# Optimization experiments

Hardware: AMD Instinct MI355X
Metric: run time of the kernel (lower is better)

The kernel has to match this reference:

```python
import jax, jax.numpy as jnp
import numpy as np

SIGMAS = (1.0, 10.0, 100.0, 1000.0)
EPS_RATIO = 1e-3  # lambda ridge term and ratio clip epsilon


def euclidsq(x, y):
    # squared pairwise Euclidean distances, [m, n]
    d = jnp.sum(x * x, axis=-1)[:, None] + jnp.sum(y * y, axis=-1)[None, :] - 2.0 * (x @ y.T)
    return jnp.maximum(d, 0.0)


def kmm_ratio(Kdede, Kdenu, lam):
    # original: inv(Kdede + lam*I) @ Kdenu @ ones == solve(A, Kdenu @ ones)
    n_de = Kdede.shape[0]
    A = Kdede + lam * jnp.eye(n_de, dtype=Kdede.dtype)
    B = jnp.sum(Kdenu, axis=1, keepdims=True)  # [n_de, 1]
    return jnp.linalg.solve(A, B)


def estimate_ratio(x_de, x_nu):
    # averaged KMM ratio over Gaussian kernels with fixed sigmas, then clip
    dsq_dede = euclidsq(x_de, x_de)
    dsq_denu = euclidsq(x_de, x_nu)
    ratio = 0.0
    for s in SIGMAS:
        inv2s2 = 1.0 / (2.0 * s * s)
        Kdede = jnp.exp(-dsq_dede * inv2s2)
        Kdenu = jnp.exp(-dsq_denu * inv2s2)
        ratio = ratio + kmm_ratio(Kdede, Kdenu, EPS_RATIO)
    ratio = ratio / len(SIGMAS)
    return jax.nn.relu(ratio) + EPS_RATIO  # clip_ratio=True


def reference(z1, z2, perm1, perm2):
    n, d = z1.shape
    z1s, z2s = z1[perm1], z2[perm2]
    # numerator ratio over full concatenated embeddings
    num_ratio = estimate_ratio(jnp.concatenate([z1, z2], axis=-1),
                               jnp.concatenate([z1s, z2s], axis=-1))
    num_ratio = 1.0 / num_ratio  # [n, 1]
    x_nu = jnp.concatenate([z2, z2], axis=-1)  # constant across samples

    def per_sample(z1_i):
        # x_de row j = concat(z1_i, z2_shuffled[j])
        x_de = jnp.concatenate([jnp.broadcast_to(z1_i, (n, d)), z2s], axis=-1)
        return jnp.sum(estimate_ratio(x_de, x_nu))

    denum_sums = jax.vmap(per_sample)(z1)  # [n]
    loss = jnp.sum(-jnp.log(num_ratio[:, 0] / denum_sums))
    return loss


def setup_inputs() -> dict:
    key = jax.random.key(0)
    k1, k2 = jax.random.split(key)
    n, d = 256, 128
    z1 = jax.random.normal(k1, (n, d), dtype=jnp.float32)
    z2 = jax.random.normal(k2, (n, d), dtype=jnp.float32)
    perm1 = jnp.arange(n, dtype=jnp.int32)
    perm2 = jnp.arange(n, dtype=jnp.int32)
    return {"z1": z1, "z2": z2, "perm1": perm1, "perm2": perm2}
```

## Files before the change

### kernel.cpp

```cpp
#include <hip/hip_runtime.h>
#include <math.h>

#define N 256
#define Dd 128

__device__ __forceinline__ double inv2s2_of(int s){
    return (s==0)?0.5:(s==1)?5.0e-3:(s==2)?5.0e-5:5.0e-7;
}

__device__ __forceinline__ void sweep32(double P[32][33], int tid){
    if (tid < 64){
        int r = tid & 31, cg_ = tid >> 5;
        for (int j = 0; j < 32; j++){
            double d    = P[j][j];
            double invd = 1.0 / d;
            double cr   = P[r][j];
            double s    = cr * invd;
            bool rj = (r == j);
            double nv[16];
            #pragma unroll
            for (int c = 0; c < 16; c++){
                int col = cg_*16 + c;
                double pj = P[j][col];
                double v  = P[r][col];
                nv[c] = rj ? ((col == j) ? -invd : v * invd)
                           : ((col == j) ? s : v - s*pj);
            }
            #pragma unroll
            for (int c = 0; c < 16; c++) P[r][cg_*16+c] = nv[c];
        }
        #pragma unroll
        for (int c = 0; c < 16; c++) P[r][cg_*16+c] = -P[r][cg_*16+c];
    }
}

__global__ void k_dist(const float* __restrict__ z1, const float* __restrict__ z2,
                       const int* __restrict__ p1, const int* __restrict__ p2,
                       double* __restrict__ S0, float* __restrict__ M4,
                       float* __restrict__ U4, double* __restrict__ bpart){
    __shared__ float Xs[16][17], Ys[16][17];
    int w = blockIdx.z;
    int tx = threadIdx.x, ty = threadIdx.y;
    int row = blockIdx.y*16 + ty, col = blockIdx.x*16 + tx;
    const float *Xb[2], *Yb[2]; const int *Xp[2], *Yp[2]; int npair = 1;
    Xb[1]=0; Yb[1]=0; Xp[0]=0; Yp[0]=0; Xp[1]=0; Yp[1]=0;
    switch(w){
        case 0: Xb[0]=z1; Yb[0]=z1; Xb[1]=z2; Yb[1]=z2; npair=2; break;
        case 1: Xb[0]=z1; Yb[0]=z1; Yp[0]=p1; Xb[1]=z2; Yb[1]=z2; Yp[1]=p2; npair=2; break;
        case 2: Xb[0]=z2; Yb[0]=z2; Xp[0]=p2; Yp[0]=p2; break;
        case 3: Xb[0]=z2; Yb[0]=z2; Xp[0]=p2; break;
        default:Xb[0]=z1; Yb[0]=z2; break;
    }
    double acc = 0.0;
    for (int p = 0; p < npair; p++){
        const float* X = Xb[p]; const float* Y = Yb[p];
        int xr = blockIdx.y*16 + ty; if (Xp[p]) xr = Xp[p][xr];
        int yr = blockIdx.x*16 + ty; if (Yp[p]) yr = Yp[p][yr];
        for (int c = 0; c < Dd; c += 16){
            __syncthreads();
            Xs[ty][tx] = X[xr*Dd + c + tx];
            Ys[ty][tx] = Y[yr*Dd + c + tx];
            __syncthreads();
            #pragma unroll
            for (int t = 0; t < 16; t++){
                float d = Xs[ty][t] - Ys[tx][t];
                acc += (double)d * (double)d;
            }
        }
    }
    int o = row*N + col;
    if (w == 0){
        #pragma unroll
        for (int s = 0; s < 4; s++){
            double v = exp(-inv2s2_of(s)*acc);
            if (row == col) v += 1.0e-3;
            S0[(size_t)(4+s)*N*N + o] = v;
        }
    } else if (w == 1){
        #pragma unroll
        for (int s = 0; s < 4; s++){
            double v = exp(-inv2s2_of(s)*acc);
            v += __shfl_down(v, 8, 16);
            v += __shfl_down(v, 4, 16);
            v += __shfl_down(v, 2, 16);
            v += __shfl_down(v, 1, 16);
            if (tx == 0) bpart[((size_t)s*N + row)*16 + blockIdx.x] = v;
        }
    } else if (w == 2){
        #pragma unroll
        for (int s = 0; s < 4; s++){
            double v = exp(-inv2s2_of(s)*acc);
            if (row == col) v += 1.0e-3;
            S0[(size_t)s*N*N + o] = v;
        }
    } else if (w == 3){
        #pragma unroll
        for (int s = 0; s < 4; s++) M4[s*N*N + o] = (float)exp(-inv2s2_of(s)*acc);
    } else {
        #pragma unroll
        for (int s = 0; s < 4; s++) U4[s*N*N + o] = (float)exp(-inv2s2_of(s)*acc);
    }
}

__global__ void k_gemm_nt(const float* __restrict__ M4, const float* __restrict__ U4,
                          double* __restrict__ Bmat, const double* __restrict__ S0,
                          double* __restrict__ Pg0, double* __restrict__ dsum){
    __shared__ float Ms[32][33], Us[32][33];
    __shared__ double P[32][33];
    int tx = threadIdx.x, ty = threadIdx.y;
    int tid = ty*16 + tx;
    if (blockIdx.z == 4){
        if (blockIdx.y != 0) return;
        int mat = blockIdx.x;
        if (mat == 0) dsum[tid] = 0.0;
        const double* S = S0 + (size_t)mat*65536;
        #pragma unroll
        for (int l = 0; l < 4; l++){
            int e = tid + l*256; P[e>>5][e&31] = S[(size_t)(e>>5)*N + (e&31)];
        }
        __syncthreads();
        sweep32(P, tid);
        __syncthreads();
        double* Pp = Pg0 + (size_t)mat*1024;
        #pragma unroll
        for (int l = 0; l < 4; l++){
            int e = tid + l*256; Pp[e] = P[e>>5][e&31];
        }
        return;
    }
    int s = blockIdx.z;
    const float* Mp = M4 + s*N*N;
    const float* Up = U4 + s*N*N;
    double* Bp = Bmat + s*N*N;
    int bj = blockIdx.y*32, bi = blockIdx.x*32;
    double a00=0, a01=0, a10=0, a11=0;
    for (int kc = 0; kc < N; kc += 32){
        __syncthreads();
        #pragma unroll
        for (int l = 0; l < 4; l++){
            int e = tid + l*256; int r = e >> 5, c = e & 31;
            Ms[r][c] = Mp[(bj+r)*N + kc + c];
            Us[r][c] = Up[(bi+r)*N + kc + c];
        }
        __syncthreads();
        #pragma unroll
        for (int k = 0; k < 32; k++){
            float x0 = Ms[2*ty][k], x1 = Ms[2*ty+1][k];
            float y0 = Us[2*tx][k], y1 = Us[2*tx+1][k];
            a00 += (double)x0*y0; a01 += (double)x0*y1;
            a10 += (double)x1*y0; a11 += (double)x1*y1;
        }
    }
    Bp[(bj+2*ty  )*N + bi+2*tx  ] = a00;
    Bp[(bj+2*ty  )*N + bi+2*tx+1] = a01;
    Bp[(bj+2*ty+1)*N + bi+2*tx  ] = a10;
    Bp[(bj+2*ty+1)*N + bi+2*tx+1] = a11;
}

__global__ void k_step(const double* __restrict__ Ssrc, double* __restrict__ Sdst,
                       const double* __restrict__ PgS, double* __restrict__ PgD, int k){
    __shared__ double Pl[32][33], EJ[32][33], Cl[32][33], El[32][33];
    int bx = blockIdx.x, mat = blockIdx.y;
    const double* S = Ssrc + (size_t)mat*65536;
    double* D = Sdst + (size_t)mat*65536;
    const double* Pp = PgS + (size_t)mat*1024;
    int tid = threadIdx.x;
    int Kb = k*32;
    if (bx < 28){
        int I = 0, b = bx;
        while (b >= I+1){ b -= I+1; I++; }
        int J = b;
        int GI = ((I < k) ? I : I + 1) * 32;
        int GJ = ((J < k) ? J : J + 1) * 32;
        int r0 = 2*(tid >> 4), c0 = 2*(tid & 15);
        double rP[4], rE[4], rEJ[4];
        #pragma unroll
        for (int l = 0; l < 4; l++){
            int e = tid + l*256; int r = e >> 5, c = e & 31;
            rP[l]  = Pp[e];
            rE[l]  = S[(size_t)(GI + r)*N + Kb + c];
            rEJ[l] = S[(size_t)(GJ + r)*N + Kb + c];
        }
        double a00 = S[(size_t)(GI+r0)*N + GJ+c0];
        double a01 = S[(size_t)(GI+r0)*N + GJ+c0+1];
        double a10 = S[(size_t)(GI+r0+1)*N + GJ+c0];
        double a11 = S[(size_t)(GI+r0+1)*N + GJ+c0+1];
        #pragma unroll
        for (int l = 0; l < 4; l++){
            int e = tid + l*256; int r = e >> 5, c = e & 31;
            Pl[r][c] = rP[l];
            El[r][c] = rE[l];
            EJ[r][c] = rEJ[l];
        }
        __syncthreads();
        #pragma unroll
        for (int l = 0; l < 4; l++){
            int e = tid + l*256; int r = e >> 5, c = e & 31;
            double acc = 0.0;
            #pragma unroll
            for (int kk = 0; kk < 32; kk++) acc += EJ[r][kk] * Pl[kk][c];
            Cl[r][c] = acc;
        }
        __syncthreads();
        #pragma unroll
        for (int kk = 0; kk < 32; kk++){
            double e0 = El[r0][kk],   e1 = El[r0+1][kk];
            double b0 = Cl[c0][kk],   b1 = Cl[c0+1][kk];
            a00 -= e0*b0; a01 -= e0*b1;
            a10 -= e1*b0; a11 -= e1*b1;
        }
        double* Dp = D + (size_t)(GI + r0)*N + GJ + c0;
        Dp[0]   = a00; Dp[1]   = a01;
        Dp[N]   = a10; Dp[N+1] = a11;
        if (I != J){
            __syncthreads();
            EJ[r0][c0]   = a00; EJ[r0][c0+1]   = a01;
            EJ[r0+1][c0] = a10; EJ[r0+1][c0+1] = a11;
            __syncthreads();
            #pragma unroll
            for (int l = 0; l < 4; l++){
                int e = tid + l*256; int r = e >> 5, c = e & 31;
                D[(size_t)(GJ + r)*N + GI + c] = EJ[c][r];
            }
        } else if (I == k && k < 7){
            __syncthreads();
            El[r0][c0]   = a00; El[r0][c0+1]   = a01;
            El[r0+1][c0] = a10; El[r0+1][c0+1] = a11;
            __syncthreads();
            sweep32(El, tid);
            __syncthreads();
            double* Pd = PgD + (size_t)mat*1024;
            #pragma unroll
            for (int l = 0; l < 4; l++){
                int e = tid + l*256; Pd[e] = El[e>>5][e&31];
            }
        }
    } else {
        int T = bx - 28;
        int GT = ((T < k) ? T : T + 1) * 32;
        double rP[4], rE[4];
        #pragma unroll
        for (int l = 0; l < 4; l++){
            int e = tid + l*256; int r = e >> 5, c = e & 31;
            rP[l] = Pp[e];
            rE[l] = S[(size_t)(GT + r)*N + Kb + c];
        }
        #pragma unroll
        for (int l = 0; l < 4; l++){
            int e = tid + l*256; int r = e >> 5, c = e & 31;
            Pl[r][c] = rP[l];
            El[r][c] = rE[l];
        }
        __syncthreads();
        #pragma unroll
        for (int l = 0; l < 4; l++){
            int e = tid + l*256; int r = e >> 5, c = e & 31;
            double acc = 0.0;
            #pragma unroll
            for (int kk = 0; kk < 32; kk++) acc += El[r][kk] * Pl[kk][c];
            Cl[r][c] = acc;
        }
        __syncthreads();
        #pragma unroll
        for (int l = 0; l < 4; l++){
            int e = tid + l*256; int r = e >> 5, c = e & 31;
            D[(size_t)(GT + r)*N + Kb + c] = Cl[r][c];
        }
        #pragma unroll
        for (int l = 0; l < 4; l++){
            int e = tid + l*256; int cc = e >> 5, rr = e & 31;
            D[(size_t)(Kb + cc)*N + GT + rr] = Cl[rr][cc];
        }
        if (T == 0){
            #pragma unroll
            for (int l = 0; l < 4; l++){
                int e = tid + l*256; int i = e >> 5, j = e & 31;
                D[(size_t)(Kb + i)*N + Kb + j] = -Pl[i][j];
            }
        }
    }
}

__global__ void k_x(const double* __restrict__ Sfin, const double* __restrict__ Bmat,
                    float* __restrict__ Xm){
    int s = blockIdx.z;
    const double* Sp = Sfin + (size_t)s*N*N;
    const double* Bp = Bmat + (size_t)s*N*N;
    float* Xp = Xm + (size_t)s*N*N;
    __shared__ double Gs[32][33], Bs[32][33];
    int tx = threadIdx.x, ty = threadIdx.y;
    int tid = ty*16 + tx;
    int bj = blockIdx.y*32, bi = blockIdx.x*32;
    double a00=0, a01=0, a10=0, a11=0;
    for (int kc = 0; kc < N; kc += 32){
        __syncthreads();
        #pragma unroll
        for (int l = 0; l < 4; l++){
            int e = tid + l*256; int r = e >> 5, c = e & 31;
            Gs[r][c] = -Sp[(size_t)(bj+r)*N + kc + c];
            Bs[r][c] = Bp[(size_t)(kc+r)*N + bi + c];
        }
        __syncthreads();
        #pragma unroll
        for (int k = 0; k < 32; k++){
            double x0 = Gs[2*ty][k], x1 = Gs[2*ty+1][k];
            double y0 = Bs[k][2*tx], y1 = Bs[k][2*tx+1];
            a00 += x0*y0; a01 += x0*y1;
            a10 += x1*y0; a11 += x1*y1;
        }
    }
    Xp[(bj+2*ty  )*N + bi+2*tx  ] = (float)a00;
    Xp[(bj+2*ty  )*N + bi+2*tx+1] = (float)a01;
    Xp[(bj+2*ty+1)*N + bi+2*tx  ] = (float)a10;
    Xp[(bj+2*ty+1)*N + bi+2*tx+1] = (float)a11;
}

__global__ void k_red(const float* __restrict__ Xm, const double* __restrict__ Sfin,
                      const double* __restrict__ bpart, double* __restrict__ dsum,
                      float* __restrict__ rnum){
    __shared__ double cp[32][33];
    __shared__ double bsh[256];
    int b = blockIdx.x, tid = threadIdx.x;
    if (b < 64){
        int bj = (b >> 3)*32, bi = (b & 7)*32;
        #pragma unroll
        for (int l = 0; l < 4; l++){
            int e = tid + l*256; int r = e >> 5, c = e & 31;
            int o = (bj + r)*N + bi + c;
            float x = Xm[0*N*N + o] + Xm[1*N*N + o] + Xm[2*N*N + o] + Xm[3*N*N + o];
            cp[r][c] = (double)fmaxf(0.25f*x, 0.f);
        }
        __syncthreads();
        if (tid < 32){
            double ssum = 0;
            #pragma unroll
            for (int r = 0; r < 32; r++) ssum += cp[r][tid];
            atomicAdd(&dsum[bi + tid], ssum);
        }
    } else {
        int s = b - 64, j = tid;
        const double* Sn = Sfin + (size_t)(4+s)*N*N;
        const double* bp = bpart + (size_t)s*N*16;
        double acc = 0;
        #pragma unroll
        for (int t = 0; t < 16; t++) acc += bp[j*16 + t];
        bsh[j] = acc;
        __syncthreads();
        double y = 0;
        for (int k = 0; k < N; k++) y -= Sn[(size_t)k*N + j] * bsh[k];
        rnum[s*N + j] = (float)y;
    }
}

__global__ void k_loss2(const double* __restrict__ dsum, const float* __restrict__ rnum,
                        float* __restrict__ out){
    __shared__ double red[256];
    int i = threadIdx.x;
    double denum = dsum[i] + (double)N * 1.0e-3;
    float ravg = 0.25f*(rnum[0*N+i] + rnum[1*N+i] + rnum[2*N+i] + rnum[3*N+i]);
    double rn = (double)fmaxf(ravg, 0.f) + 1.0e-3;
    red[i] = log(rn) + log(denum);
    __syncthreads();
    for (int st = 128; st > 0; st >>= 1){
        if (i < st) red[i] += red[i + st];
        __syncthreads();
    }
    if (i == 0) out[0] = (float)red[0];
}

extern "C" void kernel_launch(void* const* d_in, const int* in_sizes, int n_in,
                              void* d_out, int out_size, void* d_ws, size_t ws_size,
                              hipStream_t stream) {
    (void)in_sizes; (void)n_in; (void)out_size; (void)ws_size;
    const float* z1 = (const float*)d_in[0];
    const float* z2 = (const float*)d_in[1];
    const int*   p1 = (const int*)d_in[2];
    const int*   p2 = (const int*)d_in[3];
    float* out = (float*)d_out;

    char* w = (char*)d_ws;
    size_t o = 0;
    auto carve = [&](size_t bytes) -> char* {
        char* p = w + o;
        o += (bytes + 255) & ~(size_t)255;
        return p;
    };
    double* bpart = (double*)carve((size_t)4*N*16*sizeof(double));
    double* dsum  = (double*)carve((size_t)N*sizeof(double));
    float*  M4    = (float*) carve((size_t)4*N*N*sizeof(float));
    float*  U4    = (float*) carve((size_t)4*N*N*sizeof(float));
    double* Bmat  = (double*)carve((size_t)4*N*N*sizeof(double));
    float*  Xm    = (float*) carve((size_t)4*N*N*sizeof(float));
    float*  rnum  = (float*) carve((size_t)4*N*sizeof(float));
    double* S0    = (double*)carve((size_t)8*N*N*sizeof(double));
    double* S1    = (double*)carve((size_t)8*N*N*sizeof(double));
    double* Pg0   = (double*)carve((size_t)8*32*32*sizeof(double));
    double* Pg1   = (double*)carve((size_t)8*32*32*sizeof(double));

    k_dist<<<dim3(16,16,5), dim3(16,16), 0, stream>>>(z1, z2, p1, p2,
                                                      S0, M4, U4, bpart);
    k_gemm_nt<<<dim3(8,8,5), dim3(16,16), 0, stream>>>(M4, U4, Bmat, S0, Pg0, dsum);
    for (int k = 0; k < 8; k++){
        double* src = (k & 1) ? S1 : S0;
        double* dst = (k & 1) ? S0 : S1;
        double* ps  = (k & 1) ? Pg1 : Pg0;
        double* pd  = (k & 1) ? Pg0 : Pg1;
        k_step<<<dim3(35,8), dim3(256), 0, stream>>>(src, dst, ps, pd, k);
    }
    k_x<<<dim3(8,8,4), dim3(16,16), 0, stream>>>(S0, Bmat, Xm);
    k_red<<<dim3(68), dim3(256), 0, stream>>>(Xm, S0, bpart, dsum, rnum);
    k_loss2<<<dim3(1), dim3(256), 0, stream>>>(dsum, rnum, out);
}
```

Measured before the change: 434.1 us.

## Fuse final GEMM, reduction and loss into one kernel with atomic tickets

Merges k_x, k_red and k_loss2 into a single launch. Atomic ticket counters let the last block to finish a tile do the cross-sigma sum, and the last contributor overall compute the loss. This removes two kernel launches and the serialization gaps between them, at the cost of extra fences and atomics. The counters are reset in k_gemm_nt on every call.

```diff
diff --git a/kernel.cpp b/kernel.cpp
--- a/kernel.cpp
+++ b/kernel.cpp
@@ -104,7 +104,8 @@
 
 __global__ void k_gemm_nt(const float* __restrict__ M4, const float* __restrict__ U4,
                           double* __restrict__ Bmat, const double* __restrict__ S0,
-                          double* __restrict__ Pg0, double* __restrict__ dsum){
+                          double* __restrict__ Pg0, double* __restrict__ dsum,
+                          unsigned* __restrict__ tick){
     __shared__ float Ms[32][33], Us[32][33];
     __shared__ double P[32][33];
     int tx = threadIdx.x, ty = threadIdx.y;
@@ -112,7 +113,10 @@
     if (blockIdx.z == 4){
         if (blockIdx.y != 0) return;
         int mat = blockIdx.x;
-        if (mat == 0) dsum[tid] = 0.0;
+        if (mat == 0){
+            dsum[tid] = 0.0;
+            if (tid < 66) tick[tid] = 0;
+        }
         const double* S = S0 + (size_t)mat*65536;
         #pragma unroll
         for (int l = 0; l < 4; l++){
@@ -281,64 +285,78 @@
     }
 }
 
-__global__ void k_x(const double* __restrict__ Sfin, const double* __restrict__ Bmat,
-                    float* __restrict__ Xm){
-    int s = blockIdx.z;
-    const double* Sp = Sfin + (size_t)s*N*N;
-    const double* Bp = Bmat + (size_t)s*N*N;
-    float* Xp = Xm + (size_t)s*N*N;
+__global__ void __launch_bounds__(256) k_xrl(
+    const double* __restrict__ Sfin, const double* __restrict__ Bmat,
+    const double* __restrict__ bpart, float* __restrict__ Xm,
+    double* __restrict__ dsum, float* __restrict__ rnum,
+    unsigned* __restrict__ tick, float* __restrict__ out)
+{
     __shared__ double Gs[32][33], Bs[32][33];
-    int tx = threadIdx.x, ty = threadIdx.y;
-    int tid = ty*16 + tx;
-    int bj = blockIdx.y*32, bi = blockIdx.x*32;
-    double a00=0, a01=0, a10=0, a11=0;
-    for (int kc = 0; kc < N; kc += 32){
-        __syncthreads();
-        #pragma unroll
-        for (int l = 0; l < 4; l++){
-            int e = tid + l*256; int r = e >> 5, c = e & 31;
-            Gs[r][c] = -Sp[(size_t)(bj+r)*N + kc + c];
-            Bs[r][c] = Bp[(size_t)(kc+r)*N + bi + c];
-        }
-        __syncthreads();
-        #pragma unroll
-        for (int k = 0; k < 32; k++){
-            double x0 = Gs[2*ty][k], x1 = Gs[2*ty+1][k];
-            double y0 = Bs[k][2*tx], y1 = Bs[k][2*tx+1];
-            a00 += x0*y0; a01 += x0*y1;
-            a10 += x1*y0; a11 += x1*y1;
-        }
-    }
-    Xp[(bj+2*ty  )*N + bi+2*tx  ] = (float)a00;
-    Xp[(bj+2*ty  )*N + bi+2*tx+1] = (float)a01;
-    Xp[(bj+2*ty+1)*N + bi+2*tx  ] = (float)a10;
-    Xp[(bj+2*ty+1)*N + bi+2*tx+1] = (float)a11;
-}
-
-__global__ void k_red(const float* __restrict__ Xm, const double* __restrict__ Sfin,
-                      const double* __restrict__ bpart, double* __restrict__ dsum,
-                      float* __restrict__ rnum){
-    __shared__ double cp[32][33];
+    __shared__ double aux[32][33];
     __shared__ double bsh[256];
+    __shared__ unsigned shi;
     int b = blockIdx.x, tid = threadIdx.x;
-    if (b < 64){
-        int bj = (b >> 3)*32, bi = (b & 7)*32;
-        #pragma unroll
-        for (int l = 0; l < 4; l++){
-            int e = tid + l*256; int r = e >> 5, c = e & 31;
-            int o = (bj + r)*N + bi + c;
-            float x = Xm[0*N*N + o] + Xm[1*N*N + o] + Xm[2*N*N + o] + Xm[3*N*N + o];
-            cp[r][c] = (double)fmaxf(0.25f*x, 0.f);
-        }
-        __syncthreads();
-        if (tid < 32){
-            double ssum = 0;
-            #pragma unroll
-            for (int r = 0; r < 32; r++) ssum += cp[r][tid];
-            atomicAdd(&dsum[bi + tid], ssum);
+    bool runloss = false;
+    if (b < 256){
+        int s  = b >> 6, vy = (b >> 3) & 7, vx = b & 7;
+        int tx = tid & 15, ty = tid >> 4;
+        const double* Sp = Sfin + (size_t)s*N*N;
+        const double* Bp = Bmat + (size_t)s*N*N;
+        float* Xp = Xm + (size_t)s*N*N;
+        int bj = vy*32, bi = vx*32;
+        double a00=0, a01=0, a10=0, a11=0;
+        for (int kc = 0; kc < N; kc += 32){
+            __syncthreads();
+            #pragma unroll
+            for (int l = 0; l < 4; l++){
+                int e = tid + l*256; int r = e >> 5, c = e & 31;
+                Gs[r][c] = -Sp[(size_t)(bj+r)*N + kc + c];
+                Bs[r][c] = Bp[(size_t)(kc+r)*N + bi + c];
+            }
+            __syncthreads();
+            #pragma unroll
+            for (int k = 0; k < 32; k++){
+                double x0 = Gs[2*ty][k], x1 = Gs[2*ty+1][k];
+                double y0 = Bs[k][2*tx], y1 = Bs[k][2*tx+1];
+                a00 += x0*y0; a01 += x0*y1;
+                a10 += x1*y0; a11 += x1*y1;
+            }
+        }
+        Xp[(bj+2*ty  )*N + bi+2*tx  ] = (float)a00;
+        Xp[(bj+2*ty  )*N + bi+2*tx+1] = (float)a01;
+        Xp[(bj+2*ty+1)*N + bi+2*tx  ] = (float)a10;
+        Xp[(bj+2*ty+1)*N + bi+2*tx+1] = (float)a11;
+        __threadfence();
+        __syncthreads();
+        if (tid == 0)
+            shi = __hip_atomic_fetch_add(&tick[vy*8+vx], 1u,
+                                         __ATOMIC_ACQ_REL, __HIP_MEMORY_SCOPE_AGENT);
+        __syncthreads();
+        if (shi == 3){
+            #pragma unroll
+            for (int l = 0; l < 4; l++){
+                int e = tid + l*256; int r = e >> 5, c = e & 31;
+                int o = (bj + r)*N + bi + c;
+                float x = Xm[0*N*N + o] + Xm[1*N*N + o] + Xm[2*N*N + o] + Xm[3*N*N + o];
+                aux[r][c] = (double)fmaxf(0.25f*x, 0.f);
+            }
+            __syncthreads();
+            if (tid < 32){
+                double ssum = 0;
+                #pragma unroll
+                for (int r = 0; r < 32; r++) ssum += aux[r][tid];
+                atomicAdd(&dsum[bi + tid], ssum);
+            }
+            __threadfence();
+            __syncthreads();
+            if (tid == 0)
+                shi = __hip_atomic_fetch_add(&tick[64], 1u,
+                                             __ATOMIC_ACQ_REL, __HIP_MEMORY_SCOPE_AGENT);
+            __syncthreads();
+            runloss = (shi == 67);
         }
     } else {
-        int s = b - 64, j = tid;
+        int s = b - 256, j = tid;
         const double* Sn = Sfin + (size_t)(4+s)*N*N;
         const double* bp = bpart + (size_t)s*N*16;
         double acc = 0;
@@ -349,23 +367,28 @@
         double y = 0;
         for (int k = 0; k < N; k++) y -= Sn[(size_t)k*N + j] * bsh[k];
         rnum[s*N + j] = (float)y;
-    }
-}
-
-__global__ void k_loss2(const double* __restrict__ dsum, const float* __restrict__ rnum,
-                        float* __restrict__ out){
-    __shared__ double red[256];
-    int i = threadIdx.x;
-    double denum = dsum[i] + (double)N * 1.0e-3;
-    float ravg = 0.25f*(rnum[0*N+i] + rnum[1*N+i] + rnum[2*N+i] + rnum[3*N+i]);
-    double rn = (double)fmaxf(ravg, 0.f) + 1.0e-3;
-    red[i] = log(rn) + log(denum);
-    __syncthreads();
-    for (int st = 128; st > 0; st >>= 1){
-        if (i < st) red[i] += red[i + st];
-        __syncthreads();
-    }
-    if (i == 0) out[0] = (float)red[0];
+        __threadfence();
+        __syncthreads();
+        if (tid == 0)
+            shi = __hip_atomic_fetch_add(&tick[64], 1u,
+                                         __ATOMIC_ACQ_REL, __HIP_MEMORY_SCOPE_AGENT);
+        __syncthreads();
+        runloss = (shi == 67);
+    }
+    if (runloss){
+        double* red = (double*)aux;
+        int i = tid;
+        double denum = dsum[i] + (double)N * 1.0e-3;
+        float ravg = 0.25f*(rnum[0*N+i] + rnum[1*N+i] + rnum[2*N+i] + rnum[3*N+i]);
+        double rn = (double)fmaxf(ravg, 0.f) + 1.0e-3;
+        red[i] = log(rn) + log(denum);
+        __syncthreads();
+        for (int st = 128; st > 0; st >>= 1){
+            if (i < st) red[i] += red[i + st];
+            __syncthreads();
+        }
+        if (i == 0) out[0] = (float)red[0];
+    }
 }
 
 extern "C" void kernel_launch(void* const* d_in, const int* in_sizes, int n_in,
@@ -385,6 +408,7 @@
         o += (bytes + 255) & ~(size_t)255;
         return p;
     };
+    unsigned* tick = (unsigned*)carve(512);
     double* bpart = (double*)carve((size_t)4*N*16*sizeof(double));
     double* dsum  = (double*)carve((size_t)N*sizeof(double));
     float*  M4    = (float*) carve((size_t)4*N*N*sizeof(float));
@@ -399,7 +423,8 @@
 
     k_dist<<<dim3(16,16,5), dim3(16,16), 0, stream>>>(z1, z2, p1, p2,
                                                       S0, M4, U4, bpart);
-    k_gemm_nt<<<dim3(8,8,5), dim3(16,16), 0, stream>>>(M4, U4, Bmat, S0, Pg0, dsum);
+    k_gemm_nt<<<dim3(8,8,5), dim3(16,16), 0, stream>>>(M4, U4, Bmat, S0, Pg0,
+                                                       dsum, tick);
     for (int k = 0; k < 8; k++){
         double* src = (k & 1) ? S1 : S0;
         double* dst = (k & 1) ? S0 : S1;
@@ -407,7 +432,6 @@
         double* pd  = (k & 1) ? Pg0 : Pg1;
         k_step<<<dim3(35,8), dim3(256), 0, stream>>>(src, dst, ps, pd, k);
     }
-    k_x<<<dim3(8,8,4), dim3(16,16), 0, stream>>>(S0, Bmat, Xm);
-    k_red<<<dim3(68), dim3(256), 0, stream>>>(Xm, S0, bpart, dsum, rnum);
-    k_loss2<<<dim3(1), dim3(256), 0, stream>>>(dsum, rnum, out);
-}
+    k_xrl<<<dim3(260), dim3(256), 0, stream>>>(S0, Bmat, bpart, Xm,
+                                               dsum, rnum, tick, out);
+}
```

After: 446.3 us. +2.8%, slower.
